# Optimization experiments

Hardware: AMD Instinct MI355X
Metric: run time of the kernel (lower is better)

The kernel has to match this reference:

```python
import jax, jax.numpy as jnp
import numpy as np

# ---- static config (matches init_kwargs) ----
B, N_CAMS, C, H, W = 2, 6, 256, 32, 88
BEV_H = BEV_W = 100
NQ = BEV_H * BEV_W
D_PILLAR = 4
HEADS = 8
LEVELS = 3
HEAD_DIM = C // HEADS
PC_RANGE = (-51.2, -51.2, -5.0, 51.2, 51.2, 3.0)
OGFH, OGFW = 256, 704


def _make_lidar2img():
    """Plausible lidar->image projection matrices (K @ [R|t]) for 6 ring cameras."""
    mats = np.zeros((B, N_CAMS, 4, 4), np.float32)
    K = np.array([[557.0, 0.0, OGFW / 2.0], [0.0, 557.0, OGFH / 2.0], [0.0, 0.0, 1.0]], np.float64)
    for b in range(B):
        for n in range(N_CAMS):
            yaw = 2.0 * np.pi * n / N_CAMS + 0.05 * b
            fwd = np.array([np.cos(yaw), np.sin(yaw), 0.0])
            right = np.array([np.sin(yaw), -np.cos(yaw), 0.0])
            down = np.array([0.0, 0.0, -1.0])
            R = np.stack([right, down, fwd])  # lidar -> camera axes
            cam_center = np.array([1.5 * np.cos(yaw), 1.5 * np.sin(yaw), 1.8])
            t = -R @ cam_center
            P = K @ np.concatenate([R, t[:, None]], axis=1)
            mats[b, n, :3, :] = P.astype(np.float32)
            mats[b, n, 3, 3] = 1.0
    return jnp.asarray(mats)


def setup_inputs() -> dict:
    key = jax.random.key(0)
    ks = jax.random.split(key, 16)
    s = 0.02
    return {
        'imgs': jax.random.normal(ks[0], (B, N_CAMS, C, H, W), jnp.float32),
        'lidar2img': _make_lidar2img(),
        'bev_query': jax.random.normal(ks[1], (NQ, 1, C), jnp.float32) * s,
        'bev_pos': jax.random.normal(ks[2], (1, NQ, C), jnp.float32) * s,
        'cams_embeds': jax.random.normal(ks[3], (N_CAMS, C), jnp.float32) * s,
        'level_embeds': jax.random.normal(ks[4], (LEVELS, C), jnp.float32) * s,
        'w_fpn': jax.random.normal(ks[5], (LEVELS, C, C), jnp.float32) * s,
        'b_fpn': jnp.zeros((LEVELS, C), jnp.float32),
        'w_value': jax.random.normal(ks[6], (C, C), jnp.float32) * s,
        'b_value': jnp.zeros((C,), jnp.float32),
        'w_off': jax.random.normal(ks[7], (C, HEADS * LEVELS * D_PILLAR * 2), jnp.float32) * s,
        'b_off': jax.random.normal(ks[8], (HEADS * LEVELS * D_PILLAR * 2,), jnp.float32) * 0.5,
        'w_attn': jax.random.normal(ks[9], (C, HEADS * LEVELS * D_PILLAR), jnp.float32) * s,
        'b_attn': jnp.zeros((HEADS * LEVELS * D_PILLAR,), jnp.float32),
        'w_out': jax.random.normal(ks[10], (C, C), jnp.float32) * s,
        'b_out': jnp.zeros((C,), jnp.float32),
        'w_ts1': jax.random.normal(ks[11], (C, C), jnp.float32) * s,
        'b_ts1': jnp.zeros((C,), jnp.float32),
        'w_ts2': jax.random.normal(ks[12], (C, C), jnp.float32) * s,
        'b_ts2': jnp.zeros((C,), jnp.float32),
    }


def _deform_sample(v, loc, h, w):
    """Bilinear sample (grid_sample, zero padding, align_corners=False).
    v: [N, heads, h*w, dh]; loc: [N, heads, Q, 2] normalized to [0,1]. -> [N, heads, Q, dh]"""
    x = loc[..., 0] * w - 0.5
    y = loc[..., 1] * h - 0.5
    x0 = jnp.floor(x)
    y0 = jnp.floor(y)
    out = jnp.zeros(v.shape[:2] + (loc.shape[2], v.shape[-1]), v.dtype)
    for dx in (0, 1):
        for dy in (0, 1):
            xi = x0 + dx
            yi = y0 + dy
            wgt = (1.0 - jnp.abs(x - xi)) * (1.0 - jnp.abs(y - yi))
            valid = (xi >= 0) & (xi < w) & (yi >= 0) & (yi < h)
            idx = (jnp.clip(yi, 0, h - 1) * w + jnp.clip(xi, 0, w - 1)).astype(jnp.int32)
            g = jnp.take_along_axis(v, idx[..., None], axis=2)
            out = out + g * (wgt * valid)[..., None]
    return out


def _forward(imgs, lidar2img, bev_query, bev_pos, cams_embeds, level_embeds,
             w_fpn, b_fpn, w_value, b_value, w_off, b_off, w_attn, b_attn,
             w_out, b_out, w_ts1, b_ts1, w_ts2, b_ts2):
    # ---- FPN: 3 levels at strides 1/2/4 with per-level 1x1 projection ----
    x = imgs.reshape(B * N_CAMS, C, H, W)
    feats, shapes = [], []
    cur = x
    for l in range(LEVELS):
        if l > 0:
            bn, c, h, w = cur.shape
            cur = cur.reshape(bn, c, h // 2, 2, w // 2, 2).mean(axis=(3, 5))
        f = jnp.einsum('bchw,cd->bdhw', cur, w_fpn[l]) + b_fpn[l][None, :, None, None]
        feats.append(f)
        shapes.append((f.shape[2], f.shape[3]))
    # ---- flatten levels + cam/level embeds: [N, sum_hw, B, C] ----
    flat = []
    for l, f in enumerate(feats):
        h, w = shapes[l]
        fl = jnp.transpose(f.reshape(B, N_CAMS, C, h * w), (1, 0, 3, 2))  # [N,B,hw,C]
        fl = fl + cams_embeds[:, None, None, :] + level_embeds[l][None, None, None, :]
        flat.append(fl)
    feat_flatten = jnp.transpose(jnp.concatenate(flat, axis=2), (0, 2, 1, 3))  # [N,sum_hw,B,C]

    # ---- 3D pillar reference points, normalized [0,1] ----
    zrange = PC_RANGE[5] - PC_RANGE[2]
    zs = jnp.linspace(0.5, zrange - 0.5, D_PILLAR) / zrange
    xs = (jnp.arange(BEV_W, dtype=jnp.float32) + 0.5) / BEV_W
    ys = (jnp.arange(BEV_H, dtype=jnp.float32) + 0.5) / BEV_H
    gy, gx = jnp.meshgrid(ys, xs, indexing='ij')
    ref2d = jnp.stack([gx.ravel(), gy.ravel()], axis=-1)  # [NQ,2]
    ref3d = jnp.concatenate([
        jnp.broadcast_to(ref2d[None], (D_PILLAR, NQ, 2)),
        jnp.broadcast_to(zs[:, None, None].astype(jnp.float32), (D_PILLAR, NQ, 1)),
    ], axis=-1)
    scale = jnp.array([PC_RANGE[3] - PC_RANGE[0], PC_RANGE[4] - PC_RANGE[1], zrange], jnp.float32)
    shift = jnp.array(PC_RANGE[:3], jnp.float32)
    xyz = ref3d * scale + shift
    homog = jnp.concatenate([xyz, jnp.ones((D_PILLAR, NQ, 1), jnp.float32)], axis=-1)

    # ---- point sampling: project to each camera, mask invalid pixels ----
    pts = jnp.einsum('bnij,dqj->nbqdi', lidar2img, homog)  # [N,B,NQ,D,4]
    eps = 1e-5
    depth = pts[..., 2]
    xy = pts[..., :2] / jnp.maximum(depth[..., None], eps)
    ref_cam = xy / jnp.array([OGFW, OGFH], jnp.float32)  # [N,B,NQ,D,2]
    bev_mask = ((depth > eps) & (ref_cam[..., 0] > 0) & (ref_cam[..., 0] < 1)
                & (ref_cam[..., 1] > 0) & (ref_cam[..., 1] < 1))  # [N,B,NQ,D]

    pos = bev_pos[0]  # [NQ,C]

    def sca(query, value, ref_b, mask_b):
        # query [NQ,C]; value [N,sum_hw,C]; ref_b [N,NQ,D,2]; mask_b [N,NQ,D]
        residual = query
        q = query + pos
        v = value @ w_value + b_value
        off = (q @ w_off + b_off).reshape(NQ, HEADS, LEVELS, D_PILLAR, 2)
        attn = jax.nn.softmax((q @ w_attn + b_attn).reshape(NQ, HEADS, LEVELS * D_PILLAR), axis=-1)
        attn = attn.reshape(NQ, HEADS, LEVELS, D_PILLAR)
        out = jnp.zeros((N_CAMS, NQ, HEADS, HEAD_DIM), q.dtype)
        start = 0
        for l, (h, w) in enumerate(shapes):
            hw = h * w
            v_l = jnp.transpose(v[:, start:start + hw].reshape(N_CAMS, hw, HEADS, HEAD_DIM), (0, 2, 1, 3))
            start += hw
            norm = jnp.array([w, h], q.dtype)
            loc = ref_b[:, :, None, :, :] + off[None, :, :, l] / norm  # [N,NQ,heads,D,2]
            loc = jnp.transpose(loc, (0, 2, 1, 3, 4)).reshape(N_CAMS, HEADS, NQ * D_PILLAR, 2)
            s = _deform_sample(v_l, loc, h, w).reshape(N_CAMS, HEADS, NQ, D_PILLAR, HEAD_DIM)
            out = out + jnp.einsum('nhqpd,qhp->nqhd', s, attn[:, :, l])
        out = out.reshape(N_CAMS, NQ, C)
        valid = mask_b.any(axis=-1)  # [N,NQ]
        slots = (out * valid[..., None].astype(out.dtype)).sum(axis=0)
        count = jnp.maximum(valid.sum(axis=0), 1).astype(out.dtype)[:, None]
        slots = slots / count
        return slots @ w_out + b_out + residual

    def tsblock(t):
        return jax.nn.relu(t @ w_ts1 + b_ts1) @ w_ts2 + b_ts2

    bq = jnp.transpose(bev_query, (1, 0, 2))[0]  # [NQ,C]
    groups = []
    ego = bq
    for b in range(B):
        val = feat_flatten[:, :, b, :]
        r = ref_cam[:, b]
        m = bev_mask[:, b]
        if b == 0:
            for _ in range(2):
                bq = tsblock(sca(bq, val, r, m))
            ego = bq
            groups.append(ego.reshape(C, BEV_W, BEV_H))
        else:
            nb = tsblock(sca(ego, val, r, m))
            groups.append(nb.reshape(C, BEV_W, BEV_H))
    bev_groups = jnp.stack(groups, axis=0)  # [B,C,BEV_W,BEV_H]
    return bq[None], bev_groups


def reference(imgs, lidar2img, bev_query, bev_pos, cams_embeds, level_embeds,
              w_fpn, b_fpn, w_value, b_value, w_off, b_off, w_attn, b_attn,
              w_out, b_out, w_ts1, b_ts1, w_ts2, b_ts2):
    return _forward(imgs, lidar2img, bev_query, bev_pos, cams_embeds, level_embeds,
                    w_fpn, b_fpn, w_value, b_value, w_off, b_off, w_attn, b_attn,
                    w_out, b_out, w_ts1, b_ts1, w_ts2, b_ts2)
```

## Files before the change

kernel.cpp:

```cpp
#include <hip/hip_runtime.h>
#include <math.h>

typedef __attribute__((ext_vector_type(8))) short bf16x8;
typedef __attribute__((ext_vector_type(4))) float f32x4;

__device__ __forceinline__ unsigned short f2bf(float x) {
  union { float f; unsigned int u; } v; v.f = x;
  unsigned int r = v.u + 0x7fffu + ((v.u >> 16) & 1u);
  return (unsigned short)(r >> 16);
}
__device__ __forceinline__ float bf2f(unsigned short b) {
  union { unsigned int u; float f; } v; v.u = ((unsigned int)b) << 16; return v.f;
}
__device__ __forceinline__ void split2(float x, unsigned short& h, unsigned short& l) {
  h = f2bf(x);
  l = f2bf(x - bf2f(h));
}
__device__ __forceinline__ int fsi(int q, int c) { return q * 256 + (c ^ ((q & 7) << 2)); }

__device__ __forceinline__ void ld16(const unsigned short* b, bf16x8* f) {
  const unsigned short* b1 = b + 2048;
  const unsigned short* b2 = b + 4096;
  const unsigned short* b3 = b + 6144;
  asm volatile(
    "global_load_dwordx4 %0, %16, off\n\t"
    "global_load_dwordx4 %1, %16, off offset:1024\n\t"
    "global_load_dwordx4 %2, %16, off offset:2048\n\t"
    "global_load_dwordx4 %3, %16, off offset:3072\n\t"
    "global_load_dwordx4 %4, %17, off\n\t"
    "global_load_dwordx4 %5, %17, off offset:1024\n\t"
    "global_load_dwordx4 %6, %17, off offset:2048\n\t"
    "global_load_dwordx4 %7, %17, off offset:3072\n\t"
    "global_load_dwordx4 %8, %18, off\n\t"
    "global_load_dwordx4 %9, %18, off offset:1024\n\t"
    "global_load_dwordx4 %10, %18, off offset:2048\n\t"
    "global_load_dwordx4 %11, %18, off offset:3072\n\t"
    "global_load_dwordx4 %12, %19, off\n\t"
    "global_load_dwordx4 %13, %19, off offset:1024\n\t"
    "global_load_dwordx4 %14, %19, off offset:2048\n\t"
    "global_load_dwordx4 %15, %19, off offset:3072\n\t"
    "s_waitcnt vmcnt(0)"
    : "=&v"(f[0]), "=&v"(f[1]), "=&v"(f[2]), "=&v"(f[3]),
      "=&v"(f[4]), "=&v"(f[5]), "=&v"(f[6]), "=&v"(f[7]),
      "=&v"(f[8]), "=&v"(f[9]), "=&v"(f[10]), "=&v"(f[11]),
      "=&v"(f[12]), "=&v"(f[13]), "=&v"(f[14]), "=&v"(f[15])
    : "v"(b), "v"(b1), "v"(b2), "v"(b3));
}

#define MFMA(a, b, c) __builtin_amdgcn_mfma_f32_16x16x32_bf16(a, b, c, 0, 0, 0)

__device__ __forceinline__ void gemm2t32(
    const unsigned short* __restrict__ Wp, int tile0,
    int lane, int lk, int l15,
    const unsigned short (&AS)[2][32][32][8], f32x4 (&acc)[2][2])
{
  const unsigned short* base = Wp + ((size_t)(tile0 >> 1) * 16384) + (size_t)lane * 8;
  bf16x8 f[32];
  ld16(base, f);
  ld16(base + 8192, f + 16);
#pragma unroll
  for (int ks = 0; ks < 8; ++ks) {
    bf16x8 h0 = f[2 * ks], l0 = f[2 * ks + 1];
    bf16x8 h1 = f[16 + 2 * ks], l1 = f[17 + 2 * ks];
#pragma unroll
    for (int nf = 0; nf < 2; ++nf) {
      bf16x8 bqh = *(const bf16x8*)&AS[0][ks * 4 + lk][nf * 16 + l15][0];
      bf16x8 bql = *(const bf16x8*)&AS[1][ks * 4 + lk][nf * 16 + l15][0];
      acc[0][nf] = MFMA(h0, bqh, acc[0][nf]);
      acc[0][nf] = MFMA(h0, bql, acc[0][nf]);
      acc[0][nf] = MFMA(l0, bqh, acc[0][nf]);
      acc[1][nf] = MFMA(h1, bqh, acc[1][nf]);
      acc[1][nf] = MFMA(h1, bql, acc[1][nf]);
      acc[1][nf] = MFMA(l1, bqh, acc[1][nf]);
    }
  }
}

__device__ __forceinline__ void gemm2t64(
    const unsigned short* __restrict__ Wp, int tile0,
    int lane, int lk, int l15,
    const unsigned short (&AS)[2][32][64][8], f32x4 (&acc)[2][4])
{
  const unsigned short* base = Wp + ((size_t)(tile0 >> 1) * 16384) + (size_t)lane * 8;
  bf16x8 f[32];
  ld16(base, f);
  ld16(base + 8192, f + 16);
#pragma unroll
  for (int ks = 0; ks < 8; ++ks) {
    bf16x8 h0 = f[2 * ks], l0 = f[2 * ks + 1];
    bf16x8 h1 = f[16 + 2 * ks], l1 = f[17 + 2 * ks];
#pragma unroll
    for (int nf = 0; nf < 4; ++nf) {
      bf16x8 bqh = *(const bf16x8*)&AS[0][ks * 4 + lk][nf * 16 + l15][0];
      bf16x8 bql = *(const bf16x8*)&AS[1][ks * 4 + lk][nf * 16 + l15][0];
      acc[0][nf] = MFMA(h0, bqh, acc[0][nf]);
      acc[0][nf] = MFMA(h0, bql, acc[0][nf]);
      acc[0][nf] = MFMA(l0, bqh, acc[0][nf]);
      acc[1][nf] = MFMA(h1, bqh, acc[1][nf]);
      acc[1][nf] = MFMA(h1, bql, acc[1][nf]);
      acc[1][nf] = MFMA(l1, bqh, acc[1][nf]);
    }
  }
}

__device__ __forceinline__ void gemm1t64(
    const unsigned short* __restrict__ Wp, int tile,
    int lane, int lk, int l15,
    const unsigned short (&AS)[2][32][64][8], f32x4 (&acc)[4])
{
  const unsigned short* base = Wp + ((size_t)(tile >> 1) * 16384) + (size_t)(tile & 1) * 8192 + (size_t)lane * 8;
  bf16x8 f[16];
  ld16(base, f);
#pragma unroll
  for (int ks = 0; ks < 8; ++ks) {
    bf16x8 eh = f[2 * ks], el = f[2 * ks + 1];
#pragma unroll
    for (int nf = 0; nf < 4; ++nf) {
      bf16x8 bqh = *(const bf16x8*)&AS[0][ks * 4 + lk][nf * 16 + l15][0];
      bf16x8 bql = *(const bf16x8*)&AS[1][ks * 4 + lk][nf * 16 + l15][0];
      acc[nf] = MFMA(eh, bqh, acc[nf]);
      acc[nf] = MFMA(eh, bql, acc[nf]);
      acc[nf] = MFMA(el, bqh, acc[nf]);
    }
  }
}

__global__ __launch_bounds__(256) void pool2x2(const float* __restrict__ in, float* __restrict__ out,
                                               int h, int w, int total)
{
  int i = blockIdx.x * 256 + threadIdx.x;
  if (i >= total) return;
  int x = i % w; int r = i / w; int y = r % h; int ci = r / h;
  const float* p = in + (size_t)ci * (4 * h * w) + (size_t)(2 * y) * (2 * w) + 2 * x;
  out[i] = (p[0] + p[1] + p[2 * w] + p[2 * w + 1]) * 0.25f;
}

__global__ __launch_bounds__(256) void prep(
    const float* __restrict__ wo, const float* __restrict__ bo,
    const float* __restrict__ wa, const float* __restrict__ ba,
    const float* __restrict__ wout, const float* __restrict__ wts1, const float* __restrict__ wts2,
    const float* __restrict__ wfpn, const float* __restrict__ wval,
    const float* __restrict__ cams, const float* __restrict__ lev,
    const float* __restrict__ bfpn, const float* __restrict__ bval,
    unsigned short* __restrict__ wcatH, unsigned short* __restrict__ wcatL, float* __restrict__ bcat,
    unsigned short* __restrict__ woutH, unsigned short* __restrict__ woutL,
    unsigned short* __restrict__ wts1H, unsigned short* __restrict__ wts1L,
    unsigned short* __restrict__ w45H, unsigned short* __restrict__ w45L,
    unsigned short* __restrict__ wcombH, unsigned short* __restrict__ wcombL,
    float* __restrict__ e2)
{
  int bb = blockIdx.x, t = threadIdx.x;
  if (bb < 768) {
    int l = bb >> 8, i = bb & 255, j = t;
    const float* a = wfpn + ((size_t)l * 256 + i) * 256;
    float acc = 0.f;
    for (int k = 0; k < 256; ++k) acc = fmaf(a[k], wval[(size_t)k * 256 + j], acc);
    unsigned short h, lo; split2(acc, h, lo);
    size_t o = ((size_t)l * 256 + j) * 256 + i;
    wcombH[o] = h; wcombL[o] = lo;
  } else if (bb < 1056) {
    int i = (bb - 768) * 256 + t;
    int c = i >> 8, k = i & 255;
    float v = (c < 192) ? wo[k * 192 + c] : wa[k * 96 + (c - 192)];
    unsigned short h, l; split2(v, h, l);
    wcatH[i] = h; wcatL[i] = l;
    if (i < 288) bcat[i] = (i < 192) ? bo[i] : ba[i - 192];
  } else if (bb < 1312) {
    int i = (bb - 1056) * 256 + t;
    int nn = i >> 8, k = i & 255;
    float v = wout[(size_t)k * 256 + nn];
    unsigned short h, l; split2(v, h, l);
    woutH[i] = h; woutL[i] = l;
  } else if (bb < 1568) {
    int i = (bb - 1312) * 256 + t;
    int nn = i >> 8, k = i & 255;
    float v = wts1[(size_t)k * 256 + nn];
    unsigned short h, l; split2(v, h, l);
    wts1H[i] = h; wts1L[i] = l;
  } else if (bb < 1824) {
    int i = (bb - 1568) * 256 + t;
    int nn = i >> 8, k = i & 255;
    float v = wts2[(size_t)k * 256 + nn];
    unsigned short h, l; split2(v, h, l);
    w45H[i] = h; w45L[i] = l;
  } else if (bb < 2112) {
    int mp = bb - 1824;
    int k = t;
    float acc = 0.f;
    for (int j = 0; j < 256; ++j) {
      float wc = (mp < 192) ? wo[j * 192 + mp] : wa[j * 96 + (mp - 192)];
      acc = fmaf(wts2[(size_t)k * 256 + j], wc, acc);
    }
    unsigned short h, l; split2(acc, h, l);
    size_t o = (size_t)(256 + mp) * 256 + k;
    w45H[o] = h; w45L[o] = l;
  } else {
    int e = bb - 2112;
    int n = e / 3, l = e % 3, j = t;
    float acc = bval[j];
    for (int k = 0; k < 256; ++k) {
      float s = cams[n * 256 + k] + lev[l * 256 + k] + bfpn[l * 256 + k];
      acc = fmaf(s, wval[(size_t)k * 256 + j], acc);
    }
    e2[(size_t)e * 256 + j] = acc;
  }
}

__global__ __launch_bounds__(256) void relayout(
    const unsigned short* __restrict__ wcombH, const unsigned short* __restrict__ wcombL,
    const unsigned short* __restrict__ wcatH, const unsigned short* __restrict__ wcatL,
    const unsigned short* __restrict__ woutH, const unsigned short* __restrict__ woutL,
    const unsigned short* __restrict__ wts1H, const unsigned short* __restrict__ wts1L,
    const unsigned short* __restrict__ w45H, const unsigned short* __restrict__ w45L,
    unsigned short* __restrict__ wcombP, unsigned short* __restrict__ wcatP,
    unsigned short* __restrict__ woutP, unsigned short* __restrict__ wts1P,
    unsigned short* __restrict__ w45P)
{
  int bb = blockIdx.x, t = threadIdx.x;
  const unsigned short *H, *L; unsigned short* P; int tile;
  if (bb < 48)      { H = wcombH; L = wcombL; P = wcombP; tile = bb; }
  else if (bb < 66) { H = wcatH;  L = wcatL;  P = wcatP;  tile = bb - 48; }
  else if (bb < 82) { H = woutH;  L = woutL;  P = woutP;  tile = bb - 66; }
  else if (bb < 98) { H = wts1H;  L = wts1L;  P = wts1P;  tile = bb - 82; }
  else              { H = w45H;   L = w45L;   P = w45P;   tile = bb - 98; }
#pragma unroll
  for (int e = 0; e < 32; ++e) {
    int idx = t * 32 + e;
    int slot = idx >> 9;
    int lane = (idx >> 3) & 63;
    int j8 = idx & 7;
    int ks = slot >> 1, hl = slot & 1;
    int col = tile * 16 + (lane & 15);
    int k = ks * 32 + (lane >> 4) * 8 + j8;
    size_t dst = ((size_t)(tile >> 1) * 16384) + (size_t)(((tile & 1) << 4) + slot) * 512 + (size_t)lane * 8 + j8;
    P[dst] = (hl ? L : H)[(size_t)col * 256 + k];
  }
}

__global__ __launch_bounds__(512) void value_fused(
    const float* __restrict__ img0, const float* __restrict__ cur1, const float* __restrict__ cur2,
    const unsigned short* __restrict__ wcombP,
    const float* __restrict__ e2, float* __restrict__ V)
{
  __shared__ __align__(16) unsigned short AS[2][32][32][8];
  int t = threadIdx.x, wid = t >> 6, lane = t & 63, l15 = lane & 15, lk = lane >> 4;
  int bx = blockIdx.x, cam = blockIdx.y;
  int level, tb, hw; const float* src;
  if (bx < 88)       { level = 0; tb = bx;       hw = 2816; src = img0; }
  else if (bx < 110) { level = 1; tb = bx - 88;  hw = 704;  src = cur1; }
  else               { level = 2; tb = bx - 110; hw = 176;  src = cur2; }
  int p0 = tb * 32;
  const int LST[3] = {0, 2816, 3520};
  src += (size_t)cam * 256 * hw;

  {
    int f4g = t & 7, kb = t >> 3;
    bool full = (p0 + 32 <= hw);
#pragma unroll
    for (int j = 0; j < 4; ++j) {
      int k = kb + j * 64;
      const float* row = src + (size_t)k * hw;
      int p = p0 + 4 * f4g;
      float4 v;
      if (full) v = *(const float4*)(row + p);
      else {
        v.x = (p < hw) ? row[p] : 0.f;     v.y = (p + 1 < hw) ? row[p + 1] : 0.f;
        v.z = (p + 2 < hw) ? row[p + 2] : 0.f; v.w = (p + 3 < hw) ? row[p + 3] : 0.f;
      }
      int ch = k >> 3, ko = k & 7;
      unsigned short h, l;
      split2(v.x, h, l); AS[0][ch][4 * f4g + 0][ko] = h; AS[1][ch][4 * f4g + 0][ko] = l;
      split2(v.y, h, l); AS[0][ch][4 * f4g + 1][ko] = h; AS[1][ch][4 * f4g + 1][ko] = l;
      split2(v.z, h, l); AS[0][ch][4 * f4g + 2][ko] = h; AS[1][ch][4 * f4g + 2][ko] = l;
      split2(v.w, h, l); AS[0][ch][4 * f4g + 3][ko] = h; AS[1][ch][4 * f4g + 3][ko] = l;
    }
  }
  __syncthreads();

  f32x4 zed = {0.f, 0.f, 0.f, 0.f};
  f32x4 acc[2][2] = {{zed, zed}, {zed, zed}};
  gemm2t32(wcombP, level * 16 + wid * 2, lane, lk, l15, AS, acc);
  __syncthreads();

  float* ASf = (float*)(&AS[0][0][0][0]);
  const float* bias = e2 + (size_t)(cam * 3 + level) * 256;
#pragma unroll
  for (int mf = 0; mf < 2; ++mf) {
    int chb = (wid * 2 + mf) * 16 + lk * 4;
    float4 b4 = *(const float4*)(bias + chb);
#pragma unroll
    for (int nf = 0; nf < 2; ++nf) {
      int q = nf * 16 + l15;
      float4 o;
      o.x = acc[mf][nf][0] + b4.x; o.y = acc[mf][nf][1] + b4.y;
      o.z = acc[mf][nf][2] + b4.z; o.w = acc[mf][nf][3] + b4.w;
      *(float4*)&ASf[fsi(q, chb)] = o;
    }
  }
  __syncthreads();
  float* Vb = V + ((size_t)cam * 3696 + LST[level] + p0) * 256;
#pragma unroll
  for (int j = 0; j < 4; ++j) {
    int g = t + j * 512;
    int q = g >> 6, c = (g & 63) * 4;
    if (p0 + q < hw)
      *(float4*)(Vb + (size_t)q * 256 + c) = *(const float4*)&ASf[fsi(q, c)];
  }
}

__global__ __launch_bounds__(512) void fused_iter(
    const float* __restrict__ slots, const float* __restrict__ qin,
    const float* __restrict__ pos2, const float* __restrict__ rowbias,
    const unsigned short* __restrict__ woutP, const unsigned short* __restrict__ wts1P,
    const unsigned short* __restrict__ w45P, const unsigned short* __restrict__ wcatP,
    const float* __restrict__ bout, const float* __restrict__ bts1,
    const float* __restrict__ bts2, const float* __restrict__ bcat,
    float* __restrict__ qout, float* __restrict__ outA, float* __restrict__ outB,
    float* __restrict__ qtmpA, float* __restrict__ qtmpB, int init)
{
  __shared__ __align__(16) unsigned short AS[2][32][64][8];
  float* ASf = (float*)(&AS[0][0][0][0]);
  int t = threadIdx.x, wid = t >> 6, lane = t & 63, l15 = lane & 15, lk = lane >> 4;
  int r0 = blockIdx.x * 64;
  f32x4 zed = {0.f, 0.f, 0.f, 0.f};

  {
    const float* base = init ? qin : slots;
#pragma unroll
    for (int j = 0; j < 8; ++j) {
      int g = t + j * 512;
      int q = g >> 6, c = (g & 63) * 4;
      int rq = r0 + q; if (rq > 9999) rq = 9999;
      float4 a = *(const float4*)(base + (size_t)rq * 256 + c);
      if (init) {
        if (pos2) {
          float4 p = *(const float4*)(pos2 + (size_t)rq * 256 + c);
          a.x += p.x; a.y += p.y; a.z += p.z; a.w += p.w;
        }
        if (rowbias) {
          float4 rb = *(const float4*)(rowbias + c);
          a.x += rb.x; a.y += rb.y; a.z += rb.z; a.w += rb.w;
        }
      }
      ushort4 hh, ll;
      split2(a.x, hh.x, ll.x); split2(a.y, hh.y, ll.y);
      split2(a.z, hh.z, ll.z); split2(a.w, hh.w, ll.w);
      *(ushort4*)&AS[0][c >> 3][q][c & 7] = hh;
      *(ushort4*)&AS[1][c >> 3][q][c & 7] = ll;
    }
  }
  __syncthreads();

  if (init) {
    f32x4 acc[2][4] = {{zed, zed, zed, zed}, {zed, zed, zed, zed}};
    gemm2t64(wcatP, wid * 2, lane, lk, l15, AS, acc);
    f32x4 acc3[4] = {zed, zed, zed, zed};
    if (wid < 2) gemm1t64(wcatP, 16 + wid, lane, lk, l15, AS, acc3);
    __syncthreads();
#pragma unroll
    for (int mf = 0; mf < 2; ++mf) {
      int chb = (wid * 2 + mf) * 16 + lk * 4;
      float4 b4 = *(const float4*)(bcat + chb);
#pragma unroll
      for (int nf = 0; nf < 4; ++nf) {
        int q = nf * 16 + l15;
        float4 o;
        o.x = acc[mf][nf][0] + b4.x; o.y = acc[mf][nf][1] + b4.y;
        o.z = acc[mf][nf][2] + b4.z; o.w = acc[mf][nf][3] + b4.w;
        *(float4*)&ASf[fsi(q, chb)] = o;
      }
    }
    if (wid < 2) {
      int ce = wid * 16 + lk * 4;
      float4 b4 = *(const float4*)(bcat + 256 + ce);
#pragma unroll
      for (int nf = 0; nf < 4; ++nf) {
        int qg = r0 + nf * 16 + l15;
        if (qg < 10000) {
          float4 o;
          o.x = acc3[nf][0] + b4.x; o.y = acc3[nf][1] + b4.y;
          o.z = acc3[nf][2] + b4.z; o.w = acc3[nf][3] + b4.w;
          *(float4*)(qtmpB + (size_t)qg * 32 + ce) = o;
        }
      }
    }
    __syncthreads();
#pragma unroll
    for (int j = 0; j < 8; ++j) {
      int g = t + j * 512;
      int q = g >> 6, c = (g & 63) * 4;
      int qg = r0 + q;
      if (qg < 10000)
        *(float4*)(qtmpA + (size_t)qg * 256 + c) = *(const float4*)&ASf[fsi(q, c)];
    }
    return;
  }

  {
    f32x4 acc[2][4] = {{zed, zed, zed, zed}, {zed, zed, zed, zed}};
    gemm2t64(woutP, wid * 2, lane, lk, l15, AS, acc);
    __syncthreads();
    float4 qreg[8];
#pragma unroll
    for (int j = 0; j < 8; ++j) {
      int g = t + j * 512;
      int q = g >> 6, c = (g & 63) * 4;
      int rq = r0 + q; if (rq > 9999) rq = 9999;
      qreg[j] = *(const float4*)(qin + (size_t)rq * 256 + c);
    }
#pragma unroll
    for (int j = 0; j < 8; ++j) {
      int g = t + j * 512;
      int q = g >> 6, c = (g & 63) * 4;
      *(float4*)&ASf[fsi(q, c)] = qreg[j];
    }
    __syncthreads();
    float4 rr[2][4];
#pragma unroll
    for (int mf = 0; mf < 2; ++mf) {
      int chb = (wid * 2 + mf) * 16 + lk * 4;
#pragma unroll
      for (int nf = 0; nf < 4; ++nf)
        rr[mf][nf] = *(const float4*)&ASf[fsi(nf * 16 + l15, chb)];
    }
    __syncthreads();
#pragma unroll
    for (int mf = 0; mf < 2; ++mf) {
      int chb = (wid * 2 + mf) * 16 + lk * 4;
      float4 b4 = *(const float4*)(bout + chb);
#pragma unroll
      for (int nf = 0; nf < 4; ++nf) {
        int q = nf * 16 + l15;
        float v0 = acc[mf][nf][0] + b4.x + rr[mf][nf].x;
        float v1 = acc[mf][nf][1] + b4.y + rr[mf][nf].y;
        float v2 = acc[mf][nf][2] + b4.z + rr[mf][nf].z;
        float v3 = acc[mf][nf][3] + b4.w + rr[mf][nf].w;
        ushort4 hh, ll;
        split2(v0, hh.x, ll.x); split2(v1, hh.y, ll.y);
        split2(v2, hh.z, ll.z); split2(v3, hh.w, ll.w);
        *(ushort4*)&AS[0][chb >> 3][q][chb & 7] = hh;
        *(ushort4*)&AS[1][chb >> 3][q][chb & 7] = ll;
      }
    }
    __syncthreads();
  }
  {
    f32x4 acc[2][4] = {{zed, zed, zed, zed}, {zed, zed, zed, zed}};
    gemm2t64(wts1P, wid * 2, lane, lk, l15, AS, acc);
    __syncthreads();
#pragma unroll
    for (int mf = 0; mf < 2; ++mf) {
      int chb = (wid * 2 + mf) * 16 + lk * 4;
      float4 b4 = *(const float4*)(bts1 + chb);
#pragma unroll
      for (int nf = 0; nf < 4; ++nf) {
        int q = nf * 16 + l15;
        float v0 = fmaxf(acc[mf][nf][0] + b4.x, 0.f);
        float v1 = fmaxf(acc[mf][nf][1] + b4.y, 0.f);
        float v2 = fmaxf(acc[mf][nf][2] + b4.z, 0.f);
        float v3 = fmaxf(acc[mf][nf][3] + b4.w, 0.f);
        ushort4 hh, ll;
        split2(v0, hh.x, ll.x); split2(v1, hh.y, ll.y);
        split2(v2, hh.z, ll.z); split2(v3, hh.w, ll.w);
        *(ushort4*)&AS[0][chb >> 3][q][chb & 7] = hh;
        *(ushort4*)&AS[1][chb >> 3][q][chb & 7] = ll;
      }
    }
    __syncthreads();
  }
  {
    f32x4 accA[2][4] = {{zed, zed, zed, zed}, {zed, zed, zed, zed}};
    f32x4 accB[2][4] = {{zed, zed, zed, zed}, {zed, zed, zed, zed}};
    if (wid < 4 || qtmpA) {
      gemm2t64(w45P, wid * 4,     lane, lk, l15, AS, accA);
      gemm2t64(w45P, wid * 4 + 2, lane, lk, l15, AS, accB);
    }
    f32x4 acc3[4] = {zed, zed, zed, zed};
    if (qtmpA && wid < 2) gemm1t64(w45P, 32 + wid, lane, lk, l15, AS, acc3);
    __syncthreads();
    if (wid < 4) {
#pragma unroll
      for (int half = 0; half < 2; ++half) {
#pragma unroll
        for (int mf = 0; mf < 2; ++mf) {
          int chb = (wid * 4 + half * 2 + mf) * 16 + lk * 4;
          float4 b4 = *(const float4*)(bts2 + chb);
#pragma unroll
          for (int nf = 0; nf < 4; ++nf) {
            int q = nf * 16 + l15;
            f32x4 a = half ? accB[mf][nf] : accA[mf][nf];
            float4 o;
            o.x = a[0] + b4.x; o.y = a[1] + b4.y;
            o.z = a[2] + b4.z; o.w = a[3] + b4.w;
            *(float4*)&ASf[fsi(q, chb)] = o;
          }
        }
      }
    }
    if (qtmpA && wid < 2) {
      int ce = wid * 16 + lk * 4;
#pragma unroll
      for (int nf = 0; nf < 4; ++nf) {
        int qg = r0 + nf * 16 + l15;
        if (qg < 10000) {
          float4 o;
          o.x = acc3[nf][0]; o.y = acc3[nf][1]; o.z = acc3[nf][2]; o.w = acc3[nf][3];
          *(float4*)(qtmpB + (size_t)qg * 32 + ce) = o;
        }
      }
    }
    __syncthreads();
#pragma unroll
    for (int j = 0; j < 8; ++j) {
      int g = t + j * 512;
      int q = g >> 6, c = (g & 63) * 4;
      int qg = r0 + q;
      if (qg < 10000) {
        float4 vq = *(const float4*)&ASf[fsi(q, c)];
        size_t go = (size_t)qg * 256 + c;
        *(float4*)(qout + go) = vq;
        if (outA) { *(float4*)(outA + go) = vq; *(float4*)(outB + go) = vq; }
      }
    }
    if (!qtmpA) return;
    __syncthreads();
    if (wid >= 4) {
#pragma unroll
      for (int half = 0; half < 2; ++half) {
#pragma unroll
        for (int mf = 0; mf < 2; ++mf) {
          int cc = ((wid - 4) * 4 + half * 2 + mf) * 16 + lk * 4;
#pragma unroll
          for (int nf = 0; nf < 4; ++nf) {
            int q = nf * 16 + l15;
            f32x4 a = half ? accB[mf][nf] : accA[mf][nf];
            float4 o;
            o.x = a[0]; o.y = a[1]; o.z = a[2]; o.w = a[3];
            *(float4*)&ASf[fsi(q, cc)] = o;
          }
        }
      }
    }
    __syncthreads();
#pragma unroll
    for (int j = 0; j < 8; ++j) {
      int g = t + j * 512;
      int q = g >> 6, c = (g & 63) * 4;
      int qg = r0 + q;
      if (qg < 10000)
// ... 17 lines not shown
  __shared__ int mnd[24];
  __shared__ int validn[6];
  __shared__ __align__(16) float w4[576][4];
  __shared__ __align__(16) int o4[576][4];

  {
    float x = qtmpA[(size_t)q * 256 + t];
    if (posA) x += posA[(size_t)q * 256 + t];
    raw[t] = x;
    if (t < 32) {
      float y = qtmpB[(size_t)q * 32 + t];
      if (posB) y += posB[(size_t)q * 32 + t];
      raw[256 + t] = y;
    }
  }
  if (t >= 32 && t < 56) {
    int tt = t - 32;
    int n = tt >> 2, d = tt & 3;
    const float* Mrow = l2i + n * 16;
    int qx = q % 100, qy = q / 100;
    float X = ((qx + 0.5f) / 100.0f) * 102.4f + (-51.2f);
    float Y = ((qy + 0.5f) / 100.0f) * 102.4f + (-51.2f);
    float zi = (d == 3) ? 7.5f : (0.5f + (float)d * (7.0f / 3.0f));
    float Z = zi + (-5.0f);
    float px = Mrow[0] * X + Mrow[1] * Y + Mrow[2] * Z + Mrow[3];
    float py = Mrow[4] * X + Mrow[5] * Y + Mrow[6] * Z + Mrow[7];
    float pz = Mrow[8] * X + Mrow[9] * Y + Mrow[10] * Z + Mrow[11];
    float dz = fmaxf(pz, 1e-5f);
    float xc = (px / dz) / 704.0f;
    float yc = (py / dz) / 256.0f;
    refx[n][d] = xc; refy[n][d] = yc;
    mnd[n * 4 + d] = (pz > 1e-5f) && (xc > 0.f) && (xc < 1.f) && (yc > 0.f) && (yc < 1.f);
  }
  __syncthreads();
  if (t < 8) {
    float mx = raw[192 + t * 12];
    for (int p = 1; p < 12; ++p) mx = fmaxf(mx, raw[192 + t * 12 + p]);
    float s = 0.f;
    float e[12];
#pragma unroll
    for (int p = 0; p < 12; ++p) { e[p] = __expf(raw[192 + t * 12 + p] - mx); s += e[p]; }
    float inv = 1.f / s;
#pragma unroll
    for (int p = 0; p < 12; ++p) attnS[t * 12 + p] = e[p] * inv;
  } else if (t < 14) {
    int n = t - 8;
    validn[n] = mnd[n * 4] | mnd[n * 4 + 1] | mnd[n * 4 + 2] | mnd[n * 4 + 3];
  }
  __syncthreads();

  int packed = 0, nv = 0;
#pragma unroll
  for (int n = 0; n < 6; ++n)
    if (validn[n]) { packed |= n << (3 * nv); nv++; }
  float invc = 1.f / (float)(nv > 1 ? nv : 1);

  const float WWf[3] = {88.f, 44.f, 22.f}, HHf[3] = {32.f, 16.f, 8.f};
  const int WWi[3] = {88, 44, 22}, STi[3] = {0, 2816, 3520};
  int npts = nv * 96;
  for (int pt = t; pt < npts; pt += 256) {
    int hd = pt & 7;
    int g = pt >> 3;
    int j = g % 12, ni = g / 12;
    int n = (packed >> (3 * ni)) & 7;
    int l = j >> 2, d = j & 3;
    float wwf = WWf[l], hhf = HHf[l];
    int wwi = WWi[l], st = STi[l];
    float a = attnS[hd * 12 + j] * invc;
    float ox = raw[hd * 24 + l * 8 + d * 2 + 0];
    float oy = raw[hd * 24 + l * 8 + d * 2 + 1];
    float x = refx[n][d] * wwf + ox - 0.5f;
    float y = refy[n][d] * hhf + oy - 0.5f;
    float x0 = floorf(x), y0 = floorf(y);
    float fx = x - x0, fy = y - y0;
    float wx0 = 1.f - fx, wy0 = 1.f - fy;
    float vx0 = (x0 >= 0.f && x0 < wwf) ? 1.f : 0.f;
    float vx1 = (x0 + 1.f >= 0.f && x0 + 1.f < wwf) ? 1.f : 0.f;
    float vy0 = (y0 >= 0.f && y0 < hhf) ? 1.f : 0.f;
    float vy1 = (y0 + 1.f >= 0.f && y0 + 1.f < hhf) ? 1.f : 0.f;
    w4[pt][0] = a * wx0 * wy0 * vx0 * vy0;
    w4[pt][1] = a * fx * wy0 * vx1 * vy0;
    w4[pt][2] = a * wx0 * fy * vx0 * vy1;
    w4[pt][3] = a * fx * fy * vx1 * vy1;
    int ix0 = (int)fminf(fmaxf(x0, 0.f), wwf - 1.f);
    int ix1 = (int)fminf(fmaxf(x0 + 1.f, 0.f), wwf - 1.f);
    int iy0 = (int)fminf(fmaxf(y0, 0.f), hhf - 1.f);
    int iy1 = (int)fminf(fmaxf(y0 + 1.f, 0.f), hhf - 1.f);
    int rA = (st + iy0 * wwi) << 10, rB = (st + iy1 * wwi) << 10;
    o4[pt][0] = rA + (ix0 << 10);
    o4[pt][1] = rA + (ix1 << 10);
    o4[pt][2] = rB + (ix0 << 10);
    o4[pt][3] = rB + (ix1 << 10);
  }
  __syncthreads();

  int t4 = t << 2;
  float acc0 = 0.f, acc1 = 0.f;
  int sl = 0;
#pragma unroll
  for (int n = 0; n < 6; ++n) {
    if (!validn[n]) continue;
    const char* Vn = (const char*)(V + (size_t)n * 946176);
    int pb = sl * 96 + head;
    sl++;
    float va[48];
#pragma unroll
    for (int j = 0; j < 12; ++j) {
      int4 o = *reinterpret_cast<const int4*>(&o4[pb + j * 8][0]);
      va[4 * j + 0] = *(const float*)(Vn + (unsigned)(o.x + t4));
      va[4 * j + 1] = *(const float*)(Vn + (unsigned)(o.y + t4));
      va[4 * j + 2] = *(const float*)(Vn + (unsigned)(o.z + t4));
      va[4 * j + 3] = *(const float*)(Vn + (unsigned)(o.w + t4));
    }
#pragma unroll
    for (int j = 0; j < 12; ++j) {
      float4 w = *reinterpret_cast<const float4*>(&w4[pb + j * 8][0]);
      acc0 = fmaf(w.x, va[4 * j + 0], acc0);
      acc1 = fmaf(w.y, va[4 * j + 1], acc1);
      acc0 = fmaf(w.z, va[4 * j + 2], acc0);
      acc1 = fmaf(w.w, va[4 * j + 3], acc1);
    }
  }
  slots[(size_t)q * 256 + t] = acc0 + acc1;
}

extern "C" void kernel_launch(void* const* d_in, const int* in_sizes, int n_in,
                              void* d_out, int out_size, void* d_ws, size_t ws_size,
                              hipStream_t stream)
{
  const float* imgs = (const float*)d_in[0];
  const float* l2i = (const float*)d_in[1];
  const float* bev_query = (const float*)d_in[2];
  const float* bev_pos = (const float*)d_in[3];
  const float* cams = (const float*)d_in[4];
  const float* lev = (const float*)d_in[5];
  const float* wfpn = (const float*)d_in[6];
  const float* bfpn = (const float*)d_in[7];
  const float* wval = (const float*)d_in[8];
  const float* bval = (const float*)d_in[9];
  const float* woff = (const float*)d_in[10];
  const float* boff = (const float*)d_in[11];
  const float* wattn = (const float*)d_in[12];
  const float* battn = (const float*)d_in[13];
  const float* wout = (const float*)d_in[14];
  const float* bout = (const float*)d_in[15];
  const float* wts1 = (const float*)d_in[16];
  const float* bts1 = (const float*)d_in[17];
  const float* wts2 = (const float*)d_in[18];
  const float* bts2 = (const float*)d_in[19];

  float* W = (float*)d_ws;
  size_t off = 0;
  auto alloc = [&](size_t n) { float* p = W + off; off += n; return p; };
  float* v    = alloc((size_t)6 * 3696 * 256);
  float* cur1 = alloc((size_t)12 * 256 * 16 * 44);
  float* cur2 = alloc((size_t)12 * 256 * 8 * 22);
  float* bqA  = alloc(2560000);
  float* bqB  = alloc(2560000);
  float* qtmpA = alloc(2560000);
  float* qtmpB = alloc(320000);
  float* posA = alloc(2560000);
  float* posB = alloc(320000);
  float* slots = alloc(2560000);
  float* wcatR = alloc(73728);
  float* woutR = alloc(65536);
  float* wts1R = alloc(65536);
  float* w45R = alloc(139264);
  float* wcombR = alloc(196608);
  float* wcombPR = alloc(196608);
  float* wcatPR = alloc(73728);
  float* woutPR = alloc(65536);
  float* wts1PR = alloc(65536);
  float* w45PR = alloc(139264);
  float* bcat = alloc(512);
  float* e2 = alloc(4608);
  (void)ws_size; (void)in_sizes; (void)n_in; (void)out_size;

  unsigned short* wcat_h = (unsigned short*)wcatR;   unsigned short* wcat_l = wcat_h + 288 * 256;
  unsigned short* wout_h = (unsigned short*)woutR;   unsigned short* wout_l = wout_h + 65536;
  unsigned short* wts1_h = (unsigned short*)wts1R;   unsigned short* wts1_l = wts1_h + 65536;
  unsigned short* w45_h = (unsigned short*)w45R;     unsigned short* w45_l = w45_h + 544 * 256;
  unsigned short* wcomb_h = (unsigned short*)wcombR; unsigned short* wcomb_l = wcomb_h + 3 * 65536;
  unsigned short* wcombP = (unsigned short*)wcombPR;
  unsigned short* wcatP = (unsigned short*)wcatPR;
  unsigned short* woutP = (unsigned short*)woutPR;
  unsigned short* wts1P = (unsigned short*)wts1PR;
  unsigned short* w45P = (unsigned short*)w45PR;

  float* OUT = (float*)d_out;

  pool2x2<<<8448, 256, 0, stream>>>(imgs, cur1, 16, 44, 2162688);
  pool2x2<<<2112, 256, 0, stream>>>(cur1, cur2, 8, 22, 540672);
  prep<<<2130, 256, 0, stream>>>(woff, boff, wattn, battn, wout, wts1, wts2, wfpn, wval,
                                 cams, lev, bfpn, bval,
                                 wcat_h, wcat_l, bcat, wout_h, wout_l, wts1_h, wts1_l,
                                 w45_h, w45_l, wcomb_h, wcomb_l, e2);
  relayout<<<132, 256, 0, stream>>>(wcomb_h, wcomb_l, wcat_h, wcat_l, wout_h, wout_l,
                                    wts1_h, wts1_l, w45_h, w45_l,
                                    wcombP, wcatP, woutP, wts1P, w45P);

  fused_iter<<<157, 512, 0, stream>>>(nullptr, bev_pos, nullptr, bts2,
      woutP, wts1P, w45P, wcatP, bout, bts1, bts2, bcat,
      nullptr, nullptr, nullptr, posA, posB, 1);
  fused_iter<<<157, 512, 0, stream>>>(nullptr, bev_query, bev_pos, nullptr,
      woutP, wts1P, w45P, wcatP, bout, bts1, bts2, bcat,
      nullptr, nullptr, nullptr, qtmpA, qtmpB, 1);

  value_fused<<<dim3(116, 6), 512, 0, stream>>>(imgs, cur1, cur2, wcombP, e2, v);

  sca_sample<<<10000, 256, 0, stream>>>(qtmpA, qtmpB, nullptr, nullptr, v, l2i, slots);
  fused_iter<<<157, 512, 0, stream>>>(slots, bev_query, nullptr, nullptr,
      woutP, wts1P, w45P, wcatP, bout, bts1, bts2, bcat,
      bqA, nullptr, nullptr, qtmpA, qtmpB, 0);
  sca_sample<<<10000, 256, 0, stream>>>(qtmpA, qtmpB, posA, posB, v, l2i, slots);
  fused_iter<<<157, 512, 0, stream>>>(slots, bqA, nullptr, nullptr,
      woutP, wts1P, w45P, wcatP, bout, bts1, bts2, bcat,
      bqB, OUT, OUT + 2560000, qtmpA, qtmpB, 0);

  value_fused<<<dim3(116, 6), 512, 0, stream>>>(imgs + (size_t)4325376, cur1 + (size_t)1081344,
                                                cur2 + (size_t)270336, wcombP, e2, v);
  sca_sample<<<10000, 256, 0, stream>>>(qtmpA, qtmpB, posA, posB, v, l2i + 96, slots);
  fused_iter<<<157, 512, 0, stream>>>(slots, bqB, nullptr, nullptr,
      woutP, wts1P, w45P, wcatP, bout, bts1, bts2, bcat,
      OUT + 5120000, nullptr, nullptr, nullptr, nullptr, 0);
}
```

Before: 302.0 us.

## Fold weight relayout into prep, merge init and value launches across batches

Prep now writes weights directly in the packed MFMA layout, so the separate relayout kernel and the intermediate H/L buffers are gone. The two init passes through fused_iter become one init_fused launch with a 2-wide grid, and the two per-batch value_fused launches become one launch with a z dimension. The value buffer is doubled so both batches stay resident. This cuts launch count and gives each launch more blocks, at the cost of more workspace memory and scattered 2-byte writes in prep.

```diff
diff --git a/kernel.cpp b/kernel.cpp
--- a/kernel.cpp
+++ b/kernel.cpp
@@ -17,6 +17,17 @@
   l = f2bf(x - bf2f(h));
 }
 __device__ __forceinline__ int fsi(int q, int c) { return q * 256 + (c ^ ((q & 7) << 2)); }
+
+__device__ __forceinline__ void writeP(unsigned short* __restrict__ P, int col, int k,
+                                       unsigned short h, unsigned short l) {
+  int tile = col >> 4;
+  int lane = (((k >> 3) & 3) << 4) | (col & 15);
+  int ks = k >> 5, j8 = k & 7;
+  size_t base = ((size_t)(tile >> 1) * 16384) + (size_t)(((tile & 1) << 4) + ks * 2) * 512
+              + (size_t)lane * 8 + j8;
+  P[base] = h;
+  P[base + 512] = l;
+}
 
 __device__ __forceinline__ void ld16(const unsigned short* b, bf16x8* f) {
   const unsigned short* b1 = b + 2048;
@@ -142,11 +153,9 @@
     const float* __restrict__ wfpn, const float* __restrict__ wval,
     const float* __restrict__ cams, const float* __restrict__ lev,
     const float* __restrict__ bfpn, const float* __restrict__ bval,
-    unsigned short* __restrict__ wcatH, unsigned short* __restrict__ wcatL, float* __restrict__ bcat,
-    unsigned short* __restrict__ woutH, unsigned short* __restrict__ woutL,
-    unsigned short* __restrict__ wts1H, unsigned short* __restrict__ wts1L,
-    unsigned short* __restrict__ w45H, unsigned short* __restrict__ w45L,
-    unsigned short* __restrict__ wcombH, unsigned short* __restrict__ wcombL,
+    unsigned short* __restrict__ wcatP, float* __restrict__ bcat,
+    unsigned short* __restrict__ woutP, unsigned short* __restrict__ wts1P,
+    unsigned short* __restrict__ w45P, unsigned short* __restrict__ wcombP,
     float* __restrict__ e2)
 {
   int bb = blockIdx.x, t = threadIdx.x;
@@ -156,33 +165,32 @@
     float acc = 0.f;
     for (int k = 0; k < 256; ++k) acc = fmaf(a[k], wval[(size_t)k * 256 + j], acc);
     unsigned short h, lo; split2(acc, h, lo);
-    size_t o = ((size_t)l * 256 + j) * 256 + i;
-    wcombH[o] = h; wcombL[o] = lo;
+    writeP(wcombP, l * 256 + j, i, h, lo);
   } else if (bb < 1056) {
     int i = (bb - 768) * 256 + t;
     int c = i >> 8, k = i & 255;
     float v = (c < 192) ? wo[k * 192 + c] : wa[k * 96 + (c - 192)];
     unsigned short h, l; split2(v, h, l);
-    wcatH[i] = h; wcatL[i] = l;
+    writeP(wcatP, c, k, h, l);
     if (i < 288) bcat[i] = (i < 192) ? bo[i] : ba[i - 192];
   } else if (bb < 1312) {
     int i = (bb - 1056) * 256 + t;
     int nn = i >> 8, k = i & 255;
     float v = wout[(size_t)k * 256 + nn];
     unsigned short h, l; split2(v, h, l);
-    woutH[i] = h; woutL[i] = l;
+    writeP(woutP, nn, k, h, l);
   } else if (bb < 1568) {
     int i = (bb - 1312) * 256 + t;
     int nn = i >> 8, k = i & 255;
     float v = wts1[(size_t)k * 256 + nn];
     unsigned short h, l; split2(v, h, l);
-    wts1H[i] = h; wts1L[i] = l;
+    writeP(wts1P, nn, k, h, l);
   } else if (bb < 1824) {
     int i = (bb - 1568) * 256 + t;
     int nn = i >> 8, k = i & 255;
     float v = wts2[(size_t)k * 256 + nn];
     unsigned short h, l; split2(v, h, l);
-    w45H[i] = h; w45L[i] = l;
+    writeP(w45P, nn, k, h, l);
   } else if (bb < 2112) {
     int mp = bb - 1824;
     int k = t;
@@ -192,8 +200,7 @@
       acc = fmaf(wts2[(size_t)k * 256 + j], wc, acc);
     }
     unsigned short h, l; split2(acc, h, l);
-    size_t o = (size_t)(256 + mp) * 256 + k;
-    w45H[o] = h; w45L[o] = l;
+    writeP(w45P, 256 + mp, k, h, l);
   } else {
     int e = bb - 2112;
     int n = e / 3, l = e % 3, j = t;
@@ -206,45 +213,18 @@
   }
 }
 
-__global__ __launch_bounds__(256) void relayout(
-    const unsigned short* __restrict__ wcombH, const unsigned short* __restrict__ wcombL,
-    const unsigned short* __restrict__ wcatH, const unsigned short* __restrict__ wcatL,
-    const unsigned short* __restrict__ woutH, const unsigned short* __restrict__ woutL,
-    const unsigned short* __restrict__ wts1H, const unsigned short* __restrict__ wts1L,
-    const unsigned short* __restrict__ w45H, const unsigned short* __restrict__ w45L,
-    unsigned short* __restrict__ wcombP, unsigned short* __restrict__ wcatP,
-    unsigned short* __restrict__ woutP, unsigned short* __restrict__ wts1P,
-    unsigned short* __restrict__ w45P)
-{
-  int bb = blockIdx.x, t = threadIdx.x;
-  const unsigned short *H, *L; unsigned short* P; int tile;
-  if (bb < 48)      { H = wcombH; L = wcombL; P = wcombP; tile = bb; }
-  else if (bb < 66) { H = wcatH;  L = wcatL;  P = wcatP;  tile = bb - 48; }
-  else if (bb < 82) { H = woutH;  L = woutL;  P = woutP;  tile = bb - 66; }
-  else if (bb < 98) { H = wts1H;  L = wts1L;  P = wts1P;  tile = bb - 82; }
-  else              { H = w45H;   L = w45L;   P = w45P;   tile = bb - 98; }
-#pragma unroll
-  for (int e = 0; e < 32; ++e) {
-    int idx = t * 32 + e;
-    int slot = idx >> 9;
-    int lane = (idx >> 3) & 63;
-    int j8 = idx & 7;
-    int ks = slot >> 1, hl = slot & 1;
-    int col = tile * 16 + (lane & 15);
-    int k = ks * 32 + (lane >> 4) * 8 + j8;
-    size_t dst = ((size_t)(tile >> 1) * 16384) + (size_t)(((tile & 1) << 4) + slot) * 512 + (size_t)lane * 8 + j8;
-    P[dst] = (hl ? L : H)[(size_t)col * 256 + k];
-  }
-}
-
 __global__ __launch_bounds__(512) void value_fused(
-    const float* __restrict__ img0, const float* __restrict__ cur1, const float* __restrict__ cur2,
+    const float* __restrict__ imgs, const float* __restrict__ cur1a, const float* __restrict__ cur2a,
     const unsigned short* __restrict__ wcombP,
-    const float* __restrict__ e2, float* __restrict__ V)
+    const float* __restrict__ e2, float* __restrict__ Vall)
 {
   __shared__ __align__(16) unsigned short AS[2][32][32][8];
   int t = threadIdx.x, wid = t >> 6, lane = t & 63, l15 = lane & 15, lk = lane >> 4;
-  int bx = blockIdx.x, cam = blockIdx.y;
+  int bx = blockIdx.x, cam = blockIdx.y, bz = blockIdx.z;
+  const float* img0 = imgs + (size_t)bz * 4325376;
+  const float* cur1 = cur1a + (size_t)bz * 1081344;
+  const float* cur2 = cur2a + (size_t)bz * 270336;
+  float* V = Vall + (size_t)bz * 5677056;
   int level, tb, hw; const float* src;
   if (bx < 88)       { level = 0; tb = bx;       hw = 2816; src = img0; }
   else if (bx < 110) { level = 1; tb = bx - 88;  hw = 704;  src = cur1; }
@@ -308,15 +288,98 @@
   }
 }
 
+__global__ __launch_bounds__(512) void init_fused(
+    const float* __restrict__ bev_pos, const float* __restrict__ bev_query,
+    const float* __restrict__ bts2,
+    const unsigned short* __restrict__ wcatP, const float* __restrict__ bcat,
+    float* __restrict__ posA, float* __restrict__ posB,
+    float* __restrict__ qtmpA, float* __restrict__ qtmpB)
+{
+  __shared__ __align__(16) unsigned short AS[2][32][64][8];
+  float* ASf = (float*)(&AS[0][0][0][0]);
+  int t = threadIdx.x, wid = t >> 6, lane = t & 63, l15 = lane & 15, lk = lane >> 4;
+  int r0 = blockIdx.x * 64;
+  int y = blockIdx.y;
+  const float* base = y ? bev_query : bev_pos;
+  const float* padd = y ? bev_pos : nullptr;
+  const float* rb = y ? nullptr : bts2;
+  float* oA = y ? qtmpA : posA;
+  float* oB = y ? qtmpB : posB;
+  f32x4 zed = {0.f, 0.f, 0.f, 0.f};
+
+#pragma unroll
+  for (int j = 0; j < 8; ++j) {
+    int g = t + j * 512;
+    int q = g >> 6, c = (g & 63) * 4;
+    int rq = r0 + q; if (rq > 9999) rq = 9999;
+    float4 a = *(const float4*)(base + (size_t)rq * 256 + c);
+    if (padd) {
+      float4 p = *(const float4*)(padd + (size_t)rq * 256 + c);
+      a.x += p.x; a.y += p.y; a.z += p.z; a.w += p.w;
+    }
+    if (rb) {
+      float4 rv = *(const float4*)(rb + c);
+      a.x += rv.x; a.y += rv.y; a.z += rv.z; a.w += rv.w;
+    }
+    ushort4 hh, ll;
+    split2(a.x, hh.x, ll.x); split2(a.y, hh.y, ll.y);
+    split2(a.z, hh.z, ll.z); split2(a.w, hh.w, ll.w);
+    *(ushort4*)&AS[0][c >> 3][q][c & 7] = hh;
+    *(ushort4*)&AS[1][c >> 3][q][c & 7] = ll;
+  }
+  __syncthreads();
+
+  f32x4 acc[2][4] = {{zed, zed, zed, zed}, {zed, zed, zed, zed}};
+  gemm2t64(wcatP, wid * 2, lane, lk, l15, AS, acc);
+  f32x4 acc3[4] = {zed, zed, zed, zed};
+  if (wid < 2) gemm1t64(wcatP, 16 + wid, lane, lk, l15, AS, acc3);
+  __syncthreads();
+#pragma unroll
+  for (int mf = 0; mf < 2; ++mf) {
+    int chb = (wid * 2 + mf) * 16 + lk * 4;
+    float4 b4 = *(const float4*)(bcat + chb);
+#pragma unroll
+    for (int nf = 0; nf < 4; ++nf) {
+      int q = nf * 16 + l15;
+      float4 o;
+      o.x = acc[mf][nf][0] + b4.x; o.y = acc[mf][nf][1] + b4.y;
+      o.z = acc[mf][nf][2] + b4.z; o.w = acc[mf][nf][3] + b4.w;
+      *(float4*)&ASf[fsi(q, chb)] = o;
+    }
+  }
+  if (wid < 2) {
+    int ce = wid * 16 + lk * 4;
+    float4 b4 = *(const float4*)(bcat + 256 + ce);
+#pragma unroll
+    for (int nf = 0; nf < 4; ++nf) {
+      int qg = r0 + nf * 16 + l15;
+      if (qg < 10000) {
+        float4 o;
+        o.x = acc3[nf][0] + b4.x; o.y = acc3[nf][1] + b4.y;
+        o.z = acc3[nf][2] + b4.z; o.w = acc3[nf][3] + b4.w;
+        *(float4*)(oB + (size_t)qg * 32 + ce) = o;
+      }
+    }
+  }
+  __syncthreads();
+#pragma unroll
+  for (int j = 0; j < 8; ++j) {
+    int g = t + j * 512;
+    int q = g >> 6, c = (g & 63) * 4;
+    int qg = r0 + q;
+    if (qg < 10000)
+      *(float4*)(oA + (size_t)qg * 256 + c) = *(const float4*)&ASf[fsi(q, c)];
+  }
+}
+
 __global__ __launch_bounds__(512) void fused_iter(
     const float* __restrict__ slots, const float* __restrict__ qin,
-    const float* __restrict__ pos2, const float* __restrict__ rowbias,
     const unsigned short* __restrict__ woutP, const unsigned short* __restrict__ wts1P,
-    const unsigned short* __restrict__ w45P, const unsigned short* __restrict__ wcatP,
+    const unsigned short* __restrict__ w45P,
     const float* __restrict__ bout, const float* __restrict__ bts1,
-    const float* __restrict__ bts2, const float* __restrict__ bcat,
+    const float* __restrict__ bts2,
     float* __restrict__ qout, float* __restrict__ outA, float* __restrict__ outB,
-    float* __restrict__ qtmpA, float* __restrict__ qtmpB, int init)
+    float* __restrict__ qtmpA, float* __restrict__ qtmpB)
 {
   __shared__ __align__(16) unsigned short AS[2][32][64][8];
   float* ASf = (float*)(&AS[0][0][0][0]);
@@ -324,77 +387,19 @@
   int r0 = blockIdx.x * 64;
   f32x4 zed = {0.f, 0.f, 0.f, 0.f};
 
-  {
-    const float* base = init ? qin : slots;
-#pragma unroll
-    for (int j = 0; j < 8; ++j) {
-      int g = t + j * 512;
-      int q = g >> 6, c = (g & 63) * 4;
-      int rq = r0 + q; if (rq > 9999) rq = 9999;
-      float4 a = *(const float4*)(base + (size_t)rq * 256 + c);
-      if (init) {
-        if (pos2) {
-          float4 p = *(const float4*)(pos2 + (size_t)rq * 256 + c);
-          a.x += p.x; a.y += p.y; a.z += p.z; a.w += p.w;
-        }
-        if (rowbias) {
-          float4 rb = *(const float4*)(rowbias + c);
-          a.x += rb.x; a.y += rb.y; a.z += rb.z; a.w += rb.w;
-        }
-      }
-      ushort4 hh, ll;
-      split2(a.x, hh.x, ll.x); split2(a.y, hh.y, ll.y);
-      split2(a.z, hh.z, ll.z); split2(a.w, hh.w, ll.w);
-      *(ushort4*)&AS[0][c >> 3][q][c & 7] = hh;
-      *(ushort4*)&AS[1][c >> 3][q][c & 7] = ll;
-    }
-  }
-  __syncthreads();
-
-  if (init) {
-    f32x4 acc[2][4] = {{zed, zed, zed, zed}, {zed, zed, zed, zed}};
-    gemm2t64(wcatP, wid * 2, lane, lk, l15, AS, acc);
-    f32x4 acc3[4] = {zed, zed, zed, zed};
-    if (wid < 2) gemm1t64(wcatP, 16 + wid, lane, lk, l15, AS, acc3);
-    __syncthreads();
-#pragma unroll
-    for (int mf = 0; mf < 2; ++mf) {
-      int chb = (wid * 2 + mf) * 16 + lk * 4;
-      float4 b4 = *(const float4*)(bcat + chb);
-#pragma unroll
-      for (int nf = 0; nf < 4; ++nf) {
-        int q = nf * 16 + l15;
-        float4 o;
-        o.x = acc[mf][nf][0] + b4.x; o.y = acc[mf][nf][1] + b4.y;
-        o.z = acc[mf][nf][2] + b4.z; o.w = acc[mf][nf][3] + b4.w;
-        *(float4*)&ASf[fsi(q, chb)] = o;
-      }
-    }
-    if (wid < 2) {
-      int ce = wid * 16 + lk * 4;
-      float4 b4 = *(const float4*)(bcat + 256 + ce);
-#pragma unroll
-      for (int nf = 0; nf < 4; ++nf) {
-        int qg = r0 + nf * 16 + l15;
-        if (qg < 10000) {
-          float4 o;
-          o.x = acc3[nf][0] + b4.x; o.y = acc3[nf][1] + b4.y;
-          o.z = acc3[nf][2] + b4.z; o.w = acc3[nf][3] + b4.w;
-          *(float4*)(qtmpB + (size_t)qg * 32 + ce) = o;
-        }
-      }
-    }
-    __syncthreads();
-#pragma unroll
-    for (int j = 0; j < 8; ++j) {
-      int g = t + j * 512;
-      int q = g >> 6, c = (g & 63) * 4;
-      int qg = r0 + q;
-      if (qg < 10000)
-        *(float4*)(qtmpA + (size_t)qg * 256 + c) = *(const float4*)&ASf[fsi(q, c)];
-    }
-    return;
-  }
+#pragma unroll
+  for (int j = 0; j < 8; ++j) {
+    int g = t + j * 512;
+    int q = g >> 6, c = (g & 63) * 4;
+    int rq = r0 + q; if (rq > 9999) rq = 9999;
+    float4 a = *(const float4*)(slots + (size_t)rq * 256 + c);
+    ushort4 hh, ll;
+    split2(a.x, hh.x, ll.x); split2(a.y, hh.y, ll.y);
+    split2(a.z, hh.z, ll.z); split2(a.w, hh.w, ll.w);
+    *(ushort4*)&AS[0][c >> 3][q][c & 7] = hh;
+    *(ushort4*)&AS[1][c >> 3][q][c & 7] = ll;
+  }
+  __syncthreads();
 
   {
     f32x4 acc[2][4] = {{zed, zed, zed, zed}, {zed, zed, zed, zed}};
@@ -718,7 +723,7 @@
   float* W = (float*)d_ws;
   size_t off = 0;
   auto alloc = [&](size_t n) { float* p = W + off; off += n; return p; };
-  float* v    = alloc((size_t)6 * 3696 * 256);
+  float* v    = alloc((size_t)2 * 5677056);
   float* cur1 = alloc((size_t)12 * 256 * 16 * 44);
   float* cur2 = alloc((size_t)12 * 256 * 8 * 22);
   float* bqA  = alloc(2560000);
@@ -728,11 +733,6 @@
   float* posA = alloc(2560000);
   float* posB = alloc(320000);
   float* slots = alloc(2560000);
-  float* wcatR = alloc(73728);
-  float* woutR = alloc(65536);
-  float* wts1R = alloc(65536);
-  float* w45R = alloc(139264);
-  float* wcombR = alloc(196608);
   float* wcombPR = alloc(196608);
   float* wcatPR = alloc(73728);
   float* woutPR = alloc(65536);
@@ -742,51 +742,37 @@
   float* e2 = alloc(4608);
   (void)ws_size; (void)in_sizes; (void)n_in; (void)out_size;
 
-  unsigned short* wcat_h = (unsigned short*)wcatR;   unsigned short* wcat_l = wcat_h + 288 * 256;
-  unsigned short* wout_h = (unsigned short*)woutR;   unsigned short* wout_l = wout_h + 65536;
-  unsigned short* wts1_h = (unsigned short*)wts1R;   unsigned short* wts1_l = wts1_h + 65536;
-  unsigned short* w45_h = (unsigned short*)w45R;     unsigned short* w45_l = w45_h + 544 * 256;
-  unsigned short* wcomb_h = (unsigned short*)wcombR; unsigned short* wcomb_l = wcomb_h + 3 * 65536;
   unsigned short* wcombP = (unsigned short*)wcombPR;
   unsigned short* wcatP = (unsigned short*)wcatPR;
   unsigned short* woutP = (unsigned short*)woutPR;
   unsigned short* wts1P = (unsigned short*)wts1PR;
   unsigned short* w45P = (unsigned short*)w45PR;
 
+  float* v0 = v;
+  float* v1 = v + 5677056;
   float* OUT = (float*)d_out;
 
   pool2x2<<<8448, 256, 0, stream>>>(imgs, cur1, 16, 44, 2162688);
   pool2x2<<<2112, 256, 0, stream>>>(cur1, cur2, 8, 22, 540672);
   prep<<<2130, 256, 0, stream>>>(woff, boff, wattn, battn, wout, wts1, wts2, wfpn, wval,
                                  cams, lev, bfpn, bval,
-                                 wcat_h, wcat_l, bcat, wout_h, wout_l, wts1_h, wts1_l,
-                                 w45_h, w45_l, wcomb_h, wcomb_l, e2);
-  relayout<<<132, 256, 0, stream>>>(wcomb_h, wcomb_l, wcat_h, wcat_l, wout_h, wout_l,
-                                    wts1_h, wts1_l, w45_h, w45_l,
-                                    wcombP, wcatP, woutP, wts1P, w45P);
-
-  fused_iter<<<157, 512, 0, stream>>>(nullptr, bev_pos, nullptr, bts2,
-      woutP, wts1P, w45P, wcatP, bout, bts1, bts2, bcat,
-      nullptr, nullptr, nullptr, posA, posB, 1);
-  fused_iter<<<157, 512, 0, stream>>>(nullptr, bev_query, bev_pos, nullptr,
-      woutP, wts1P, w45P, wcatP, bout, bts1, bts2, bcat,
-      nullptr, nullptr, nullptr, qtmpA, qtmpB, 1);
-
-  value_fused<<<dim3(116, 6), 512, 0, stream>>>(imgs, cur1, cur2, wcombP, e2, v);
-
-  sca_sample<<<10000, 256, 0, stream>>>(qtmpA, qtmpB, nullptr, nullptr, v, l2i, slots);
-  fused_iter<<<157, 512, 0, stream>>>(slots, bev_query, nullptr, nullptr,
-      woutP, wts1P, w45P, wcatP, bout, bts1, bts2, bcat,
-      bqA, nullptr, nullptr, qtmpA, qtmpB, 0);
-  sca_sample<<<10000, 256, 0, stream>>>(qtmpA, qtmpB, posA, posB, v, l2i, slots);
-  fused_iter<<<157, 512, 0, stream>>>(slots, bqA, nullptr, nullptr,
-      woutP, wts1P, w45P, wcatP, bout, bts1, bts2, bcat,
-      bqB, OUT, OUT + 2560000, qtmpA, qtmpB, 0);
-
-  value_fused<<<dim3(116, 6), 512, 0, stream>>>(imgs + (size_t)4325376, cur1 + (size_t)1081344,
-                                                cur2 + (size_t)270336, wcombP, e2, v);
-  sca_sample<<<10000, 256, 0, stream>>>(qtmpA, qtmpB, posA, posB, v, l2i + 96, slots);
-  fused_iter<<<157, 512, 0, stream>>>(slots, bqB, nullptr, nullptr,
-      woutP, wts1P, w45P, wcatP, bout, bts1, bts2, bcat,
-      OUT + 5120000, nullptr, nullptr, nullptr, nullptr, 0);
-}
+                                 wcatP, bcat, woutP, wts1P, w45P, wcombP, e2);
+
+  init_fused<<<dim3(157, 2), 512, 0, stream>>>(bev_pos, bev_query, bts2, wcatP, bcat,
+                                               posA, posB, qtmpA, qtmpB);
+
+  value_fused<<<dim3(116, 6, 2), 512, 0, stream>>>(imgs, cur1, cur2, wcombP, e2, v);
+
+  sca_sample<<<10000, 256, 0, stream>>>(qtmpA, qtmpB, nullptr, nullptr, v0, l2i, slots);
+  fused_iter<<<157, 512, 0, stream>>>(slots, bev_query,
+      woutP, wts1P, w45P, bout, bts1, bts2,
+      bqA, nullptr, nullptr, qtmpA, qtmpB);
+  sca_sample<<<10000, 256, 0, stream>>>(qtmpA, qtmpB, posA, posB, v0, l2i, slots);
+  fused_iter<<<157, 512, 0, stream>>>(slots, bqA,
+      woutP, wts1P, w45P, bout, bts1, bts2,
+      bqB, OUT, OUT + 2560000, qtmpA, qtmpB);
+  sca_sample<<<10000, 256, 0, stream>>>(qtmpA, qtmpB, posA, posB, v1, l2i + 96, slots);
+  fused_iter<<<157, 512, 0, stream>>>(slots, bqB,
+      woutP, wts1P, w45P, bout, bts1, bts2,
+      OUT + 5120000, nullptr, nullptr, nullptr, nullptr);
+}
```

New measurement: 284.1 us. -5.9%, faster.
